# Performance work log

Hardware: AMD Instinct MI355X
Metric: run time of the kernel (lower is better)

Reference implementation:

```python
import jax, jax.numpy as jnp
import numpy as np

N0, N1, N2 = 1200000, 120000, 12000  # nodes per hop (outermost -> seeds)
E0, E1 = 1200000, 120000
IN_C, HID_C, OUT_C = 256, 256, 64


def setup_inputs() -> dict:
    key = jax.random.key(0)
    ks = jax.random.split(key, 10)
    s_in, s_hid = 1.0 / np.sqrt(IN_C), 1.0 / np.sqrt(HID_C)
    return {
        "x": jax.random.normal(ks[0], (N0, IN_C), dtype=jnp.float32),
        "src0": jax.random.randint(ks[1], (E0,), 0, N0, dtype=jnp.int64),
        "dst0": jax.random.randint(ks[2], (E0,), 0, N1, dtype=jnp.int64),
        "src1": jax.random.randint(ks[3], (E1,), 0, N1, dtype=jnp.int64),
        "dst1": jax.random.randint(ks[4], (E1,), 0, N2, dtype=jnp.int64),
        "Wl0": jax.random.normal(ks[5], (HID_C, IN_C), dtype=jnp.float32) * s_in,
        "b0": jnp.zeros((HID_C,), dtype=jnp.float32),
        "Wr0": jax.random.normal(ks[6], (HID_C, IN_C), dtype=jnp.float32) * s_in,
        "Wl1": jax.random.normal(ks[7], (OUT_C, HID_C), dtype=jnp.float32) * s_hid,
        "b1": jnp.zeros((OUT_C,), dtype=jnp.float32),
        "Wr1": jax.random.normal(ks[8], (OUT_C, HID_C), dtype=jnp.float32) * s_hid,
    }


def _sage_conv(x_src, x_tgt, src, dst, Wl, b, Wr, n_tgt):
    # gather neighbor (source) features, mean-scatter onto targets
    msg = x_src[src]                                          # [E, C]
    agg = jax.ops.segment_sum(msg, dst, num_segments=n_tgt)   # [n_tgt, C]
    cnt = jax.ops.segment_sum(jnp.ones((dst.shape[0],), x_src.dtype), dst,
                              num_segments=n_tgt)
    agg = agg / jnp.maximum(cnt, 1.0)[:, None]
    return agg @ Wl.T + b + x_tgt @ Wr.T


def reference(x, src0, dst0, src1, dst1, Wl0, b0, Wr0, Wl1, b1, Wr1):
    # layer 0 (eval mode: dropout is identity)
    h = _sage_conv(x, x[:N1], src0, dst0, Wl0, b0, Wr0, N1)
    h = jax.nn.relu(h)
    # layer 1
    out = _sage_conv(h, h[:N2], src1, dst1, Wl1, b1, Wr1, N2)
    return jax.nn.log_softmax(out, axis=-1)
```

## Files before the change

### kernel.cpp

```cpp
#include <hip/hip_runtime.h>
#include <stdint.h>

#define N0c 1200000
#define N1c 120000
#define N2c 12000
#define E0c 1200000
#define E1c 120000
#define NB0 118
#define NB1 12
#define N1pad 120064
#define N2pad 12032
#define ROWB 80
#define ROWU 40
#define HB 5157
#define WCB 768

typedef short short8 __attribute__((ext_vector_type(8)));
typedef float f32x4 __attribute__((ext_vector_type(4)));
typedef unsigned short u16;

__device__ __forceinline__ u16 f2bf(float f) {
    union { float f; unsigned u; } v; v.f = f;
    unsigned r = v.u + 0x7FFFu + ((v.u >> 16) & 1u);
    return (u16)(r >> 16);
}

__device__ __forceinline__ void gload16(const char* g, char* l) {
    __builtin_amdgcn_global_load_lds(
        (const __attribute__((address_space(1))) void*)g,
        (__attribute__((address_space(3))) void*)l, 16, 0, 0);
}

__global__ void k_hist(const int* __restrict__ dst0, const int* __restrict__ dst1,
                       int* __restrict__ c0, int* __restrict__ c1,
                       u16* __restrict__ Bt0, const float* __restrict__ Wl0,
                       const float* __restrict__ Wr0, u16* __restrict__ Bt1,
                       const float* __restrict__ Wl1, const float* __restrict__ Wr1) {
    if (blockIdx.x < HB) {
        int i = blockIdx.x * 256 + threadIdx.x;
        int part = blockIdx.x & 7;
        if (i < E0c) atomicAdd(&c0[part * N1c + dst0[i]], 1);
        else if (i < E0c + E1c) atomicAdd(&c1[part * N2c + dst1[i - E0c]], 1);
    } else {
        int i = (blockIdx.x - HB) * 256 + threadIdx.x;
        if (i < 256 * 512) {
            int c = i >> 9, k = i & 511;
            float v = (k < 256) ? Wl0[c * 256 + k] : Wr0[c * 256 + (k - 256)];
            Bt0[((size_t)(k >> 5) * 256 + c) * ROWU + (k & 31)] = f2bf(v);
        } else {
            int j = i - 256 * 512;
            int c = j >> 9, k = j & 511;
            float v = 0.f;
            if (c < 64) v = (k < 256) ? Wl1[c * 256 + k] : Wr1[c * 256 + (k - 256)];
            Bt1[j] = f2bf(v);
        }
    }
}

__global__ void k_scanA(const int* __restrict__ c0, const int* __restrict__ c1,
                        int* __restrict__ partials) {
    __shared__ int sh[256];
    int hop = blockIdx.x >= NB0;
    int blk = hop ? blockIdx.x - NB0 : blockIdx.x;
    const int* c = hop ? c1 : c0;
    int n = hop ? N2c : N1c;
    int d0 = blk * 1024 + threadIdx.x * 4;
    int tsum = 0;
#pragma unroll
    for (int j = 0; j < 4; ++j) {
        int d = d0 + j;
        if (d < n)
#pragma unroll
            for (int k = 0; k < 8; ++k) tsum += c[k * n + d];
    }
    sh[threadIdx.x] = tsum;
    __syncthreads();
    for (int ofs = 128; ofs > 0; ofs >>= 1) {
        if (threadIdx.x < ofs) sh[threadIdx.x] += sh[threadIdx.x + ofs];
        __syncthreads();
    }
    if (threadIdx.x == 0) partials[blockIdx.x] = sh[0];
}

__global__ void k_scanC(const int* __restrict__ c0, const int* __restrict__ c1,
                        const int* __restrict__ partials, int* __restrict__ rs0,
                        int* __restrict__ rs1, int* __restrict__ bs0,
                        int* __restrict__ bs1) {
    __shared__ int sh[256];
    __shared__ int baseSh;
    int hop = blockIdx.x >= NB0;
    int blk = hop ? blockIdx.x - NB0 : blockIdx.x;
    const int* c = hop ? c1 : c0;
    int* rs = hop ? rs1 : rs0;
    int* bs = hop ? bs1 : bs0;
    int n = hop ? N2c : N1c;
    int segBase = hop ? NB0 : 0;
    int tid = threadIdx.x;

    sh[tid] = (tid < blk) ? partials[segBase + tid] : 0;
    __syncthreads();
    for (int ofs = 128; ofs > 0; ofs >>= 1) {
        if (tid < ofs) sh[tid] += sh[tid + ofs];
        __syncthreads();
    }
    if (tid == 0) baseSh = sh[0];
    __syncthreads();

    int d0 = blk * 1024 + tid * 4;
    int cv[4][8];
    int tsum = 0;
#pragma unroll
    for (int j = 0; j < 4; ++j)
#pragma unroll
        for (int k = 0; k < 8; ++k) {
            int d = d0 + j;
            int v = (d < n) ? c[k * n + d] : 0;
            cv[j][k] = v; tsum += v;
        }
    sh[tid] = tsum; __syncthreads();
    for (int ofs = 1; ofs < 256; ofs <<= 1) {
        int t = tid >= ofs ? sh[tid - ofs] : 0;
        __syncthreads();
        sh[tid] += t;
        __syncthreads();
    }
    int run = baseSh + sh[tid] - tsum;
#pragma unroll
    for (int j = 0; j < 4; ++j) {
        int d = d0 + j;
        if (d < n) {
            rs[d] = run;
#pragma unroll
            for (int k = 0; k < 8; ++k) { bs[k * n + d] = run; run += cv[j][k]; }
        }
    }
    if (blk == 0 && tid == 0) {
        if (hop) rs1[N2c] = E1c; else rs0[N1c] = E0c;
    }
}

__global__ void k_scat(const int* __restrict__ src0, const int* __restrict__ dst0,
                       const int* __restrict__ src1, const int* __restrict__ dst1,
                       int* __restrict__ c0, int* __restrict__ c1,
                       const int* __restrict__ bs0, const int* __restrict__ bs1,
                       int* __restrict__ eidx0, int* __restrict__ eidx1) {
    int i = blockIdx.x * 256 + threadIdx.x;
    int part = blockIdx.x & 7;
    if (i < E0c) {
        int d = dst0[i];
        int off = atomicSub(&c0[part * N1c + d], 1) - 1;
        eidx0[bs0[part * N1c + d] + off] = src0[i];
    } else if (i < E0c + E1c) {
        int j = i - E0c;
        int d = dst1[j];
        int off = atomicSub(&c1[part * N2c + d], 1) - 1;
        eidx1[bs1[part * N2c + d] + off] = src1[j];
    }
}

__global__ void k_agg0(const float* __restrict__ x, const int* __restrict__ eidx,
                       const int* __restrict__ rs, u16* __restrict__ A, int ntgt) {
    int w = (int)((blockIdx.x * blockDim.x + threadIdx.x) >> 6);
    int lane = threadIdx.x & 63;
    if (w >= ntgt) return;
    int s = rs[w], e = rs[w + 1];
    float a0 = 0.f, a1 = 0.f, a2 = 0.f, a3 = 0.f;
    int i = s;
    for (; i + 8 <= e; i += 8) {
        f32x4 v[8];
#pragma unroll
        for (int u = 0; u < 8; ++u)
            v[u] = __builtin_nontemporal_load(
                ((const f32x4*)(x + (long)eidx[i + u] * 256)) + lane);
#pragma unroll
        for (int u = 0; u < 8; ++u) {
            a0 += v[u][0]; a1 += v[u][1]; a2 += v[u][2]; a3 += v[u][3];
        }
    }
    for (; i + 2 <= e; i += 2) {
        f32x4 v0 = __builtin_nontemporal_load(
            ((const f32x4*)(x + (long)eidx[i] * 256)) + lane);
        f32x4 v1 = __builtin_nontemporal_load(
            ((const f32x4*)(x + (long)eidx[i + 1] * 256)) + lane);
        a0 += v0[0] + v1[0]; a1 += v0[1] + v1[1];
        a2 += v0[2] + v1[2]; a3 += v0[3] + v1[3];
    }
    if (i < e) {
        f32x4 v = __builtin_nontemporal_load(
            ((const f32x4*)(x + (long)eidx[i] * 256)) + lane);
        a0 += v[0]; a1 += v[1]; a2 += v[2]; a3 += v[3];
    }
    int c = e - s; if (c < 1) c = 1;
    float sc = 1.f / (float)c;
    int kt = lane >> 3;
    int cu = (lane & 7) * 4;
    ushort4 oa;
    oa.x = f2bf(a0 * sc); oa.y = f2bf(a1 * sc); oa.z = f2bf(a2 * sc); oa.w = f2bf(a3 * sc);
    *(ushort4*)(A + ((size_t)kt * N1pad + w) * ROWU + cu) = oa;
}

__global__ void k_agg1(const u16* __restrict__ hsrc, const int* __restrict__ eidx,
                       const int* __restrict__ rs, u16* __restrict__ A, int ntgt) {
    int w = (int)((blockIdx.x * blockDim.x + threadIdx.x) >> 6);
    int lane = threadIdx.x & 63;
    if (w >= ntgt) return;
    int s = rs[w], e = rs[w + 1];
    float a0 = 0.f, a1 = 0.f, a2 = 0.f, a3 = 0.f;
    auto acc4 = [&](ushort4 v) {
        union { unsigned u; float f; } c0, c1, c2, c3;
        c0.u = (unsigned)v.x << 16; c1.u = (unsigned)v.y << 16;
        c2.u = (unsigned)v.z << 16; c3.u = (unsigned)v.w << 16;
        a0 += c0.f; a1 += c1.f; a2 += c2.f; a3 += c3.f;
    };
    int i = s;
    for (; i + 4 <= e; i += 4) {
        ushort4 v0 = ((const ushort4*)(hsrc + (long)eidx[i] * 256))[lane];
        ushort4 v1 = ((const ushort4*)(hsrc + (long)eidx[i + 1] * 256))[lane];
        ushort4 v2 = ((const ushort4*)(hsrc + (long)eidx[i + 2] * 256))[lane];
        ushort4 v3 = ((const ushort4*)(hsrc + (long)eidx[i + 3] * 256))[lane];
        acc4(v0); acc4(v1); acc4(v2); acc4(v3);
    }
    for (; i < e; ++i) {
        ushort4 v = ((const ushort4*)(hsrc + (long)eidx[i] * 256))[lane];
        acc4(v);
    }
    int c = e - s; if (c < 1) c = 1;
    float sc = 1.f / (float)c;
    ushort4 o;
    o.x = f2bf(a0 * sc); o.y = f2bf(a1 * sc); o.z = f2bf(a2 * sc); o.w = f2bf(a3 * sc);
    *(ushort4*)(A + (long)w * 512 + lane * 4) = o;
    ushort4 sv = ((const ushort4*)(hsrc + (long)w * 256))[lane];
    *(ushort4*)(A + (long)w * 512 + 256 + lane * 4) = sv;
}

__global__ __launch_bounds__(512)
void k_gemm0(const u16* __restrict__ A0, const float* __restrict__ x,
             const u16* __restrict__ Bt, const float* __restrict__ bias,
             u16* __restrict__ outp) {
    __shared__ int4 Lbuf[2 * 30720 / 16];
    char* L = (char*)Lbuf;
    const int tid = threadIdx.x;
    const int lane = tid & 63, wid = tid >> 6;
    const int wm = wid >> 2, wn = wid & 3;
    const long m0 = (long)blockIdx.x * 128;

    f32x4 acc[4][4];
#pragma unroll
    for (int i = 0; i < 4; ++i)
#pragma unroll
        for (int j = 0; j < 4; ++j) acc[i][j] = (f32x4){0.f, 0.f, 0.f, 0.f};

    const char* Abase = (const char*)A0 + m0 * ROWB;
    const char* Bbase = (const char*)Bt;
    const int srow = tid >> 2, scq = tid & 3;

    auto stage = [&](int buf, int kt) {
        char* lb = L + buf * 30720;
        const char* gb = Bbase + (size_t)kt * (256 * ROWB);
        if (kt < 8) {
            const char* ga = Abase + (size_t)kt * ((size_t)N1pad * ROWB);
#pragma unroll
            for (int c0 = 0; c0 < 4; ++c0) {
                int c = wid + c0 * 8;
                if (c < 30) {
                    const char* g = (c < 10) ? (ga + c * 1024) : (gb + (c - 10) * 1024);
                    gload16(g + lane * 16, lb + c * 1024);
                }
            }
        } else {
#pragma unroll
            for (int c0 = 0; c0 < 3; ++c0) {
                int c = wid + c0 * 8;
                if (c < 20) gload16(gb + c * 1024 + lane * 16, lb + 10240 + c * 1024);
            }
            const f32x4* p =
                (const f32x4*)(x + (m0 + srow) * 256 + (kt - 8) * 32 + scq * 8);
            f32x4 v0 = p[0], v1 = p[1];
            ushort4 h0, h1;
            h0.x = f2bf(v0[0]); h0.y = f2bf(v0[1]); h0.z = f2bf(v0[2]); h0.w = f2bf(v0[3]);
            h1.x = f2bf(v1[0]); h1.y = f2bf(v1[1]); h1.z = f2bf(v1[2]); h1.w = f2bf(v1[3]);
            ushort4* d = (ushort4*)(lb + srow * ROWB + scq * 16);
            d[0] = h0; d[1] = h1;
        }
    };

    stage(0, 0);
    const int rr = lane & 15, gg = lane >> 4;
    for (int ks = 0; ks < 16; ++ks) {
        int cur = ks & 1;
        __syncthreads();
        if (ks + 1 < 16) stage(cur ^ 1, ks + 1);
        const char* lb = L + cur * 30720;
        short8 af[4], bv[4];
#pragma unroll
        for (int f = 0; f < 4; ++f) {
            af[f] = *(const short8*)(lb + (wm * 64 + f * 16 + rr) * ROWB + gg * 16);
            bv[f] = *(const short8*)(lb + 10240 + (wn * 64 + f * 16 + rr) * ROWB + gg * 16);
        }
#pragma unroll
        for (int i = 0; i < 4; ++i)
#pragma unroll
            for (int j = 0; j < 4; ++j)
                acc[i][j] =
                    __builtin_amdgcn_mfma_f32_16x16x32_bf16(af[i], bv[j], acc[i][j], 0, 0, 0);
    }

#pragma unroll
    for (int j = 0; j < 4; ++j) {
        int col = wn * 64 + j * 16 + rr;
        float bvl = bias[col];
#pragma unroll
        for (int i = 0; i < 4; ++i) {
            long row = m0 + wm * 64 + i * 16 + gg * 4;
#pragma unroll
            for (int q = 0; q < 4; ++q) {
                long r = row + q;
                if (r < N1c) {
                    float v = acc[i][j][q] + bvl;
                    v = v > 0.f ? v : 0.f;
                    outp[r * 256 + col] = f2bf(v);
                }
            }
        }
    }
}

__global__ __launch_bounds__(256)
void k_gemm1(const u16* __restrict__ A, const u16* __restrict__ Bt,
             const float* __restrict__ bias, float* __restrict__ outp) {
    __shared__ u16 As[128 * 40];
    __shared__ u16 Bs[128 * 40];
    const int tid = threadIdx.x;
    const int lane = tid & 63, wid = tid >> 6;
    const int wm = wid >> 1, wn = wid & 1;
    const long m0 = (long)blockIdx.x * 128;
    const int sar = tid >> 1, sac = (tid & 1) * 16;

    f32x4 acc[4][4];
#pragma unroll
    for (int i = 0; i < 4; ++i)
#pragma unroll
        for (int j = 0; j < 4; ++j) acc[i][j] = (f32x4){0.f, 0.f, 0.f, 0.f};

    int4 ra[2]; int4 rb[2];
    auto load_tile = [&](int ks) {
        int k0 = ks * 32;
        const int4* p = (const int4*)(A + (m0 + sar) * 512 + k0 + sac);
        ra[0] = p[0]; ra[1] = p[1];
        const int4* q = (const int4*)(Bt + (long)sar * 512 + k0 + sac);
        rb[0] = q[0]; rb[1] = q[1];
    };
    auto write_tile = [&]() {
        int4* da = (int4*)(As + sar * 40 + sac);
        da[0] = ra[0]; da[1] = ra[1];
        int4* db = (int4*)(Bs + sar * 40 + sac);
        db[0] = rb[0]; db[1] = rb[1];
    };

    load_tile(0);
    for (int ks = 0; ks < 16; ++ks) {
        __syncthreads();
        write_tile();
        __syncthreads();
        if (ks + 1 < 16) load_tile(ks + 1);
        short8 af[4], bv[4];
        const int rr = lane & 15, gg = lane >> 4;
#pragma unroll
        for (int f = 0; f < 4; ++f) {
            af[f] = *(const short8*)(As + (wm * 64 + f * 16 + rr) * 40 + gg * 8);
            bv[f] = *(const short8*)(Bs + (wn * 64 + f * 16 + rr) * 40 + gg * 8);
        }
#pragma unroll
        for (int i = 0; i < 4; ++i)
#pragma unroll
            for (int j = 0; j < 4; ++j)
                acc[i][j] =
                    __builtin_amdgcn_mfma_f32_16x16x32_bf16(af[i], bv[j], acc[i][j], 0, 0, 0);
    }

    const int rr = lane & 15, gg = lane >> 4;
    if (wn == 0) {
#pragma unroll
        for (int i = 0; i < 4; ++i) {
#pragma unroll
            for (int q = 0; q < 4; ++q) {
                long r = m0 + wm * 64 + i * 16 + gg * 4 + q;
                float v[4];
#pragma unroll
                for (int j = 0; j < 4; ++j) v[j] = acc[i][j][q] + bias[j * 16 + rr];
                float mx = fmaxf(fmaxf(v[0], v[1]), fmaxf(v[2], v[3]));
#pragma unroll
                for (int m = 1; m < 16; m <<= 1) mx = fmaxf(mx, __shfl_xor(mx, m, 16));
                float se = __expf(v[0] - mx) + __expf(v[1] - mx) +
                           __expf(v[2] - mx) + __expf(v[3] - mx);
#pragma unroll
                for (int m = 1; m < 16; m <<= 1) se += __shfl_xor(se, m, 16);
                float ln = __logf(se);
                if (r < N2c) {
#pragma unroll
                    for (int j = 0; j < 4; ++j)
                        outp[r * 64 + j * 16 + rr] = v[j] - mx - ln;
                }
            }
        }
    }
}

extern "C" void kernel_launch(void* const* d_in, const int* in_sizes, int n_in,
                              void* d_out, int out_size, void* d_ws, size_t ws_size,
                              hipStream_t stream) {
    const float* x   = (const float*)d_in[0];
    const int* src0  = (const int*)d_in[1];
    const int* dst0  = (const int*)d_in[2];
    const int* src1  = (const int*)d_in[3];
    const int* dst1  = (const int*)d_in[4];
    const float* Wl0 = (const float*)d_in[5];
    const float* b0  = (const float*)d_in[6];
    const float* Wr0 = (const float*)d_in[7];
    const float* Wl1 = (const float*)d_in[8];
    const float* b1  = (const float*)d_in[9];
    const float* Wr1 = (const float*)d_in[10];

    char* base = (char*)d_ws;
    size_t off = 0;
    auto alloc = [&](size_t bytes) -> void* {
        off = (off + 255) & ~(size_t)255;
        void* p = base + off;
        off += bytes;
        return p;
    };
    int* c0       = (int*)alloc((size_t)8 * N1c * 4);
    int* c1       = (int*)alloc((size_t)8 * N2c * 4);
    int* bs0      = (int*)alloc((size_t)8 * N1c * 4);
    int* bs1      = (int*)alloc((size_t)8 * N2c * 4);
    int* rs0      = (int*)alloc((size_t)(N1c + 1) * 4);
    int* rs1      = (int*)alloc((size_t)(N2c + 1) * 4);
    int* partials = (int*)alloc((size_t)(NB0 + NB1) * 4);
    int* eidx0    = (int*)alloc((size_t)E0c * 4);
    int* eidx1    = (int*)alloc((size_t)E1c * 4);
    u16* A0       = (u16*)alloc((size_t)8 * N1pad * ROWU * 2);
    u16* hbuf     = (u16*)alloc((size_t)N1pad * 256 * 2);
    u16* A1       = (u16*)alloc((size_t)N2pad * 512 * 2);
    u16* Bt0      = (u16*)alloc((size_t)16 * 256 * ROWU * 2);
    u16* Bt1      = (u16*)alloc((size_t)128 * 512 * 2);

    (void)hipMemsetAsync(c0, 0, (size_t)8 * (N1c + N2c) * 4, stream);

    k_hist<<<HB + WCB, 256, 0, stream>>>(dst0, dst1, c0, c1,
                                         Bt0, Wl0, Wr0, Bt1, Wl1, Wr1);
    k_scanA<<<NB0 + NB1, 256, 0, stream>>>(c0, c1, partials);
    k_scanC<<<NB0 + NB1, 256, 0, stream>>>(c0, c1, partials, rs0, rs1, bs0, bs1);
    k_scat<<<HB, 256, 0, stream>>>(src0, dst0, src1, dst1,
                                   c0, c1, bs0, bs1, eidx0, eidx1);

    k_agg0<<<(N1c + 3) / 4, 256, 0, stream>>>(x, eidx0, rs0, A0, N1c);
    k_gemm0<<<N1pad / 128, 512, 0, stream>>>(A0, x, Bt0, b0, hbuf);

    k_agg1<<<(N2c + 3) / 4, 256, 0, stream>>>(hbuf, eidx1, rs1, A1, N2c);
    k_gemm1<<<N2pad / 128, 256, 0, stream>>>(A1, Bt1, b1, (float*)d_out);
}
```

Before: 528.9 us.

## Fuse CSR build stages into one cooperative kernel with grid syncs

Merges the counter memset, histogram plus weight conversion, the two scan passes and the edge scatter into a single cooperative kernel of 1024 blocks. Grid-stride loops replace the per-element launches, and grid.sync separates the phases. This removes four kernel launches and one memset, along with their launch gaps, from the preprocessing chain. In exchange it adds grid-wide barrier costs. The scan phases also run on only 130 of the 1024 blocks, leaving the rest idle there.

```diff
diff --git a/kernel.cpp b/kernel.cpp
--- a/kernel.cpp
+++ b/kernel.cpp
@@ -1,5 +1,8 @@
 #include <hip/hip_runtime.h>
+#include <hip/hip_cooperative_groups.h>
 #include <stdint.h>
+
+namespace cg = cooperative_groups;
 
 #define N0c 1200000
 #define N1c 120000
@@ -12,8 +15,7 @@
 #define N2pad 12032
 #define ROWB 80
 #define ROWU 40
-#define HB 5157
-#define WCB 768
+#define CSRB 1024
 
 typedef short short8 __attribute__((ext_vector_type(8)));
 typedef float f32x4 __attribute__((ext_vector_type(4)));
@@ -31,130 +33,128 @@
         (__attribute__((address_space(3))) void*)l, 16, 0, 0);
 }
 
-__global__ void k_hist(const int* __restrict__ dst0, const int* __restrict__ dst1,
-                       int* __restrict__ c0, int* __restrict__ c1,
-                       u16* __restrict__ Bt0, const float* __restrict__ Wl0,
-                       const float* __restrict__ Wr0, u16* __restrict__ Bt1,
-                       const float* __restrict__ Wl1, const float* __restrict__ Wr1) {
-    if (blockIdx.x < HB) {
-        int i = blockIdx.x * 256 + threadIdx.x;
-        int part = blockIdx.x & 7;
-        if (i < E0c) atomicAdd(&c0[part * N1c + dst0[i]], 1);
-        else if (i < E0c + E1c) atomicAdd(&c1[part * N2c + dst1[i - E0c]], 1);
-    } else {
-        int i = (blockIdx.x - HB) * 256 + threadIdx.x;
-        if (i < 256 * 512) {
-            int c = i >> 9, k = i & 511;
-            float v = (k < 256) ? Wl0[c * 256 + k] : Wr0[c * 256 + (k - 256)];
-            Bt0[((size_t)(k >> 5) * 256 + c) * ROWU + (k & 31)] = f2bf(v);
-        } else {
-            int j = i - 256 * 512;
-            int c = j >> 9, k = j & 511;
-            float v = 0.f;
-            if (c < 64) v = (k < 256) ? Wl1[c * 256 + k] : Wr1[c * 256 + (k - 256)];
-            Bt1[j] = f2bf(v);
-        }
-    }
-}
-
-__global__ void k_scanA(const int* __restrict__ c0, const int* __restrict__ c1,
-                        int* __restrict__ partials) {
-    __shared__ int sh[256];
-    int hop = blockIdx.x >= NB0;
-    int blk = hop ? blockIdx.x - NB0 : blockIdx.x;
-    const int* c = hop ? c1 : c0;
-    int n = hop ? N2c : N1c;
-    int d0 = blk * 1024 + threadIdx.x * 4;
-    int tsum = 0;
-#pragma unroll
-    for (int j = 0; j < 4; ++j) {
-        int d = d0 + j;
-        if (d < n)
-#pragma unroll
-            for (int k = 0; k < 8; ++k) tsum += c[k * n + d];
-    }
-    sh[threadIdx.x] = tsum;
-    __syncthreads();
-    for (int ofs = 128; ofs > 0; ofs >>= 1) {
-        if (threadIdx.x < ofs) sh[threadIdx.x] += sh[threadIdx.x + ofs];
-        __syncthreads();
-    }
-    if (threadIdx.x == 0) partials[blockIdx.x] = sh[0];
-}
-
-__global__ void k_scanC(const int* __restrict__ c0, const int* __restrict__ c1,
-                        const int* __restrict__ partials, int* __restrict__ rs0,
-                        int* __restrict__ rs1, int* __restrict__ bs0,
-                        int* __restrict__ bs1) {
+__global__ void k_csr(const int* __restrict__ src0, const int* __restrict__ dst0,
+                      const int* __restrict__ src1, const int* __restrict__ dst1,
+                      int* __restrict__ c0, int* __restrict__ c1,
+                      int* __restrict__ partials,
+                      int* __restrict__ rs0, int* __restrict__ rs1,
+                      int* __restrict__ bs0, int* __restrict__ bs1,
+                      int* __restrict__ eidx0, int* __restrict__ eidx1,
+                      u16* __restrict__ Bt0, const float* __restrict__ Wl0,
+                      const float* __restrict__ Wr0, u16* __restrict__ Bt1,
+                      const float* __restrict__ Wl1, const float* __restrict__ Wr1) {
+    cg::grid_group grid = cg::this_grid();
     __shared__ int sh[256];
     __shared__ int baseSh;
-    int hop = blockIdx.x >= NB0;
-    int blk = hop ? blockIdx.x - NB0 : blockIdx.x;
-    const int* c = hop ? c1 : c0;
-    int* rs = hop ? rs1 : rs0;
-    int* bs = hop ? bs1 : bs0;
-    int n = hop ? N2c : N1c;
-    int segBase = hop ? NB0 : 0;
-    int tid = threadIdx.x;
-
-    sh[tid] = (tid < blk) ? partials[segBase + tid] : 0;
-    __syncthreads();
-    for (int ofs = 128; ofs > 0; ofs >>= 1) {
-        if (tid < ofs) sh[tid] += sh[tid + ofs];
-        __syncthreads();
-    }
-    if (tid == 0) baseSh = sh[0];
-    __syncthreads();
-
-    int d0 = blk * 1024 + tid * 4;
-    int cv[4][8];
-    int tsum = 0;
-#pragma unroll
-    for (int j = 0; j < 4; ++j)
-#pragma unroll
-        for (int k = 0; k < 8; ++k) {
+    const int bid = blockIdx.x, tid = threadIdx.x;
+    const int part = bid & 7;
+    const int gstep = CSRB * 256;
+    const int g0 = bid * 256 + tid;
+
+    for (int i = g0; i < 8 * N1c; i += gstep) c0[i] = 0;
+    for (int i = g0; i < 8 * N2c; i += gstep) c1[i] = 0;
+    grid.sync();
+
+    for (int i = g0; i < E0c; i += gstep) atomicAdd(&c0[part * N1c + dst0[i]], 1);
+    for (int i = g0; i < E1c; i += gstep) atomicAdd(&c1[part * N2c + dst1[i]], 1);
+    for (int i = g0; i < 256 * 512; i += gstep) {
+        int c = i >> 9, k = i & 511;
+        float v = (k < 256) ? Wl0[c * 256 + k] : Wr0[c * 256 + (k - 256)];
+        Bt0[((size_t)(k >> 5) * 256 + c) * ROWU + (k & 31)] = f2bf(v);
+    }
+    for (int j = g0; j < 128 * 512; j += gstep) {
+        int c = j >> 9, k = j & 511;
+        float v = 0.f;
+        if (c < 64) v = (k < 256) ? Wl1[c * 256 + k] : Wr1[c * 256 + (k - 256)];
+        Bt1[j] = f2bf(v);
+    }
+    grid.sync();
+
+    if (bid < NB0 + NB1) {
+        int hop = bid >= NB0;
+        int blk = hop ? bid - NB0 : bid;
+        const int* c = hop ? c1 : c0;
+        int n = hop ? N2c : N1c;
+        int d0 = blk * 1024 + tid * 4;
+        int tsum = 0;
+#pragma unroll
+        for (int j = 0; j < 4; ++j) {
             int d = d0 + j;
-            int v = (d < n) ? c[k * n + d] : 0;
-            cv[j][k] = v; tsum += v;
-        }
-    sh[tid] = tsum; __syncthreads();
-    for (int ofs = 1; ofs < 256; ofs <<= 1) {
-        int t = tid >= ofs ? sh[tid - ofs] : 0;
-        __syncthreads();
-        sh[tid] += t;
-        __syncthreads();
-    }
-    int run = baseSh + sh[tid] - tsum;
-#pragma unroll
-    for (int j = 0; j < 4; ++j) {
-        int d = d0 + j;
-        if (d < n) {
-            rs[d] = run;
-#pragma unroll
-            for (int k = 0; k < 8; ++k) { bs[k * n + d] = run; run += cv[j][k]; }
-        }
-    }
-    if (blk == 0 && tid == 0) {
-        if (hop) rs1[N2c] = E1c; else rs0[N1c] = E0c;
-    }
-}
-
-__global__ void k_scat(const int* __restrict__ src0, const int* __restrict__ dst0,
-                       const int* __restrict__ src1, const int* __restrict__ dst1,
-                       int* __restrict__ c0, int* __restrict__ c1,
-                       const int* __restrict__ bs0, const int* __restrict__ bs1,
-                       int* __restrict__ eidx0, int* __restrict__ eidx1) {
-    int i = blockIdx.x * 256 + threadIdx.x;
-    int part = blockIdx.x & 7;
-    if (i < E0c) {
+            if (d < n)
+#pragma unroll
+                for (int k = 0; k < 8; ++k) tsum += c[k * n + d];
+        }
+        sh[tid] = tsum;
+        __syncthreads();
+        for (int ofs = 128; ofs > 0; ofs >>= 1) {
+            if (tid < ofs) sh[tid] += sh[tid + ofs];
+            __syncthreads();
+        }
+        if (tid == 0) partials[bid] = sh[0];
+    }
+    grid.sync();
+
+    if (bid < NB0 + NB1) {
+        int hop = bid >= NB0;
+        int blk = hop ? bid - NB0 : bid;
+        const int* c = hop ? c1 : c0;
+        int* rs = hop ? rs1 : rs0;
+        int* bs = hop ? bs1 : bs0;
+        int n = hop ? N2c : N1c;
+        int segBase = hop ? NB0 : 0;
+
+        sh[tid] = (tid < blk) ? partials[segBase + tid] : 0;
+        __syncthreads();
+        for (int ofs = 128; ofs > 0; ofs >>= 1) {
+            if (tid < ofs) sh[tid] += sh[tid + ofs];
+            __syncthreads();
+        }
+        if (tid == 0) baseSh = sh[0];
+        __syncthreads();
+
+        int d0 = blk * 1024 + tid * 4;
+        int cv[4][8];
+        int tsum = 0;
+#pragma unroll
+        for (int j = 0; j < 4; ++j)
+#pragma unroll
+            for (int k = 0; k < 8; ++k) {
+                int d = d0 + j;
+                int v = (d < n) ? c[k * n + d] : 0;
+                cv[j][k] = v; tsum += v;
+            }
+        sh[tid] = tsum; __syncthreads();
+        for (int ofs = 1; ofs < 256; ofs <<= 1) {
+            int t = tid >= ofs ? sh[tid - ofs] : 0;
+            __syncthreads();
+            sh[tid] += t;
+            __syncthreads();
+        }
+        int run = baseSh + sh[tid] - tsum;
+#pragma unroll
+        for (int j = 0; j < 4; ++j) {
+            int d = d0 + j;
+            if (d < n) {
+                rs[d] = run;
+#pragma unroll
+                for (int k = 0; k < 8; ++k) { bs[k * n + d] = run; run += cv[j][k]; }
+            }
+        }
+        if (blk == 0 && tid == 0) {
+            if (hop) rs1[N2c] = E1c; else rs0[N1c] = E0c;
+        }
+    }
+    grid.sync();
+
+    for (int i = g0; i < E0c; i += gstep) {
         int d = dst0[i];
         int off = atomicSub(&c0[part * N1c + d], 1) - 1;
         eidx0[bs0[part * N1c + d] + off] = src0[i];
-    } else if (i < E0c + E1c) {
-        int j = i - E0c;
-        int d = dst1[j];
+    }
+    for (int i = g0; i < E1c; i += gstep) {
+        int d = dst1[i];
         int off = atomicSub(&c1[part * N2c + d], 1) - 1;
-        eidx1[bs1[part * N2c + d] + off] = src1[j];
+        eidx1[bs1[part * N2c + d] + off] = src1[i];
     }
 }
 
@@ -444,14 +444,16 @@
     u16* Bt0      = (u16*)alloc((size_t)16 * 256 * ROWU * 2);
     u16* Bt1      = (u16*)alloc((size_t)128 * 512 * 2);
 
-    (void)hipMemsetAsync(c0, 0, (size_t)8 * (N1c + N2c) * 4, stream);
-
-    k_hist<<<HB + WCB, 256, 0, stream>>>(dst0, dst1, c0, c1,
-                                         Bt0, Wl0, Wr0, Bt1, Wl1, Wr1);
-    k_scanA<<<NB0 + NB1, 256, 0, stream>>>(c0, c1, partials);
-    k_scanC<<<NB0 + NB1, 256, 0, stream>>>(c0, c1, partials, rs0, rs1, bs0, bs1);
-    k_scat<<<HB, 256, 0, stream>>>(src0, dst0, src1, dst1,
-                                   c0, c1, bs0, bs1, eidx0, eidx1);
+    void* args[] = {
+        (void*)&src0, (void*)&dst0, (void*)&src1, (void*)&dst1,
+        (void*)&c0, (void*)&c1, (void*)&partials,
+        (void*)&rs0, (void*)&rs1, (void*)&bs0, (void*)&bs1,
+        (void*)&eidx0, (void*)&eidx1,
+        (void*)&Bt0, (void*)&Wl0, (void*)&Wr0,
+        (void*)&Bt1, (void*)&Wl1, (void*)&Wr1,
+    };
+    (void)hipLaunchCooperativeKernel((const void*)k_csr, dim3(CSRB), dim3(256),
+                                     args, 0, stream);
 
     k_agg0<<<(N1c + 3) / 4, 256, 0, stream>>>(x, eidx0, rs0, A0, N1c);
     k_gemm0<<<N1pad / 128, 512, 0, stream>>>(A0, x, Bt0, b0, hbuf);
```

Measured after the change: 963.8 us. +82.2%, slower.
